# Performance work log

Hardware: AMD Instinct MI355X
Metric: run time of the kernel (lower is better)

## Reference

```python
import jax, jax.numpy as jnp
import numpy as np

N, D, K = 8192, 2048, 10000
EPS = 1e-12
COMMITMENT_COST = 0.25


def _l2_normalize(v, axis):
    # matches torch F.normalize(p=2): v / max(||v||, eps)
    n = jnp.linalg.norm(v, axis=axis, keepdims=True)
    return v / jnp.maximum(n, EPS)


def setup_inputs() -> dict:
    key = jax.random.key(0)
    kx, kw = jax.random.split(key)
    x = jax.random.normal(kx, (N, D), dtype=jnp.float32)
    # nn.Embedding weight initialized uniform(0, 3) per the module
    weight = jax.random.uniform(kw, (K, D), dtype=jnp.float32, minval=0.0, maxval=3.0)
    return {"x": x, "weight": weight}


def reference(x, weight):
    # --- get_code_indices ---
    xn = _l2_normalize(x, axis=1)          # [N, D]
    wn = _l2_normalize(weight, axis=1)     # [K, D]
    # ||xn||^2 + ||wn||^2 - 2 xn . wn  -> [N, K]
    distances = (
        jnp.sum(xn * xn, axis=1, keepdims=True)
        + jnp.sum(wn * wn, axis=1)
        - 2.0 * jnp.matmul(xn, wn.T)
    )
    encoding_indices = jnp.argmin(distances, axis=1)  # [N]
    # --- quantize (gathers the UN-normalized codebook, as in the module) ---
    quantized = weight[encoding_indices]              # [N, D]
    # --- training losses ---
    q_latent_loss = jnp.mean((quantized - jax.lax.stop_gradient(x)) ** 2)
    e_latent_loss = jnp.mean((x - jax.lax.stop_gradient(quantized)) ** 2)
    loss = q_latent_loss + COMMITMENT_COST * e_latent_loss
    # straight-through estimator
    quantized = x + jax.lax.stop_gradient(quantized - x)
    return quantized, loss, encoding_indices
```

## Files before the change

### kernel.cpp

```cpp
#include <hip/hip_runtime.h>
#include <math.h>

typedef unsigned short ushort_t;
typedef short short8 __attribute__((ext_vector_type(8)));
typedef float f32x4  __attribute__((ext_vector_type(4)));

#define N_ROWS 8192
#define D_DIM  2048
#define K_CODES 10000
#define EPSF   1e-12f

#define BMT 256
#define BKT 64
#define NT_K 32
#define MTILES 32
#define NTILES 40
#define NGROUP 320

#define BAND_ADD  2e-5f
#define FBIG 1e30f

__device__ __forceinline__ unsigned short f2bf(float f) {
  unsigned u = __float_as_uint(f);
  unsigned r = (u + 0x7fffu + ((u >> 16) & 1u)) >> 16;
  return (unsigned short)r;
}
__device__ __forceinline__ float bf2f(unsigned short h) {
  return __uint_as_float(((unsigned)h) << 16);
}

__device__ __forceinline__ void stage16(const ushort_t* g, ushort_t* l) {
  __builtin_amdgcn_global_load_lds(
      (const __attribute__((address_space(1))) unsigned int*)g,
      (__attribute__((address_space(3))) unsigned int*)l, 16, 0, 0);
}

__device__ __forceinline__ float block_reduce_sum(float v) {
  #pragma unroll
  for (int o = 32; o > 0; o >>= 1) v += __shfl_down(v, o, 64);
  __shared__ float ls[4];
  int lane = threadIdx.x & 63;
  int wid  = threadIdx.x >> 6;
  if (lane == 0) ls[wid] = v;
  __syncthreads();
  v = (threadIdx.x < 4) ? ls[threadIdx.x] : 0.0f;
  if (wid == 0) {
    v += __shfl_down(v, 2, 64);
    v += __shfl_down(v, 1, 64);
  }
  __syncthreads();
  return v;
}

__global__ __launch_bounds__(256) void norm_hi_kernel(
    const float* __restrict__ src, ushort_t* __restrict__ hi,
    float* __restrict__ sq_out, float* __restrict__ inv_out,
    float* __restrict__ hn_out, float* __restrict__ ln_out)
{
  int row = blockIdx.x;
  int tid = threadIdx.x;
  const float* rp = src + (size_t)row * D_DIM;
  float4 v0 = *(const float4*)(rp + tid * 8);
  float4 v1 = *(const float4*)(rp + tid * 8 + 4);
  float s = v0.x*v0.x + v0.y*v0.y + v0.z*v0.z + v0.w*v0.w
          + v1.x*v1.x + v1.y*v1.y + v1.z*v1.z + v1.w*v1.w;
  s = block_reduce_sum(s);
  __shared__ float sh_inv;
  if (tid == 0) sh_inv = 1.0f / fmaxf(sqrtf(s), EPSF);
  __syncthreads();
  float inv = sh_inv;

  float xs[8] = {v0.x, v0.y, v0.z, v0.w, v1.x, v1.y, v1.z, v1.w};
  unsigned short hb[8];
  float t = 0.0f, th = 0.0f, tl = 0.0f;
  #pragma unroll
  for (int i = 0; i < 8; ++i) {
    float xn = xs[i] * inv;
    t += xn * xn;
    unsigned short h = f2bf(xn);
    hb[i] = h;
    float hf = bf2f(h);
    th += hf * hf;
    float l = xn - hf;
    tl += l * l;
  }
  *(short8*)(hi + (size_t)row * D_DIM + tid * 8) = *(short8*)hb;
  t  = block_reduce_sum(t);
  if (tid == 0) sq_out[row] = t;
  th = block_reduce_sum(th);
  if (tid == 0) hn_out[row] = sqrtf(th);
  tl = block_reduce_sum(tl);
  if (tid == 0) { ln_out[row] = sqrtf(tl); inv_out[row] = inv; }
}

__global__ __launch_bounds__(256) void wmax_kernel(
    const float* __restrict__ whn, const float* __restrict__ wln,
    float* __restrict__ wmax_out)
{
  int tid = threadIdx.x;
  float mh = 0.0f, ml = 0.0f;
  for (int k = tid; k < K_CODES; k += 256) {
    mh = fmaxf(mh, whn[k]);
    ml = fmaxf(ml, wln[k]);
  }
  __shared__ float sh[256], sl[256];
  sh[tid] = mh; sl[tid] = ml;
  __syncthreads();
  #pragma unroll
  for (int o = 128; o > 0; o >>= 1) {
    if (tid < o) {
      sh[tid] = fmaxf(sh[tid], sh[tid + o]);
      sl[tid] = fmaxf(sl[tid], sl[tid + o]);
    }
    __syncthreads();
  }
  if (tid == 0) { wmax_out[0] = sh[0]; wmax_out[1] = sl[0]; }
}

#define LEXLT(da, ia, db, ib) ((da) < (db) || ((da) == (db) && (ia) < (ib)))

#define READ_A(mh) { \
  _Pragma("unroll") for (int mi = 0; mi < 4; ++mi) \
  _Pragma("unroll") for (int kc = 0; kc < 2; ++kc) { \
    int r = (mh)*128 + wr*64 + mi*16 + t16; \
    int sl = (kc*4 + h4) ^ (r & 7); \
    af[mi][kc] = *(const short8*)&lA[buf][r*64 + sl*8]; } }

#define READ_B(nh, DST) { \
  _Pragma("unroll") for (int ni = 0; ni < 2; ++ni) \
  _Pragma("unroll") for (int kc = 0; kc < 2; ++kc) { \
    int r = (nh)*128 + wc*32 + ni*16 + t16; \
    int sl = (kc*4 + h4) ^ (r & 7); \
    DST[ni][kc] = *(const short8*)&lB[buf][r*64 + sl*8]; } }

#define MFMA_Q(mh, nh, BF) { \
  _Pragma("unroll") for (int mi = 0; mi < 4; ++mi) \
  _Pragma("unroll") for (int ni = 0; ni < 2; ++ni) \
  _Pragma("unroll") for (int kc = 0; kc < 2; ++kc) \
    acc[(mh)*4+mi][(nh)*2+ni] = __builtin_amdgcn_mfma_f32_16x16x32_bf16( \
        af[mi][kc], BF[ni][kc], acc[(mh)*4+mi][(nh)*2+ni], 0, 0, 0); }

#define STAGE_A(BF, HH, KKO) { \
  stage16(Ah + (size_t)(row0 + (HH)*128 + prow0) * D_DIM + (KKO) + lsl, \
          lA[BF] + (HH)*8192 + c0*512); \
  stage16(Ah + (size_t)(row0 + (HH)*128 + prow1) * D_DIM + (KKO) + lsl, \
          lA[BF] + (HH)*8192 + c0*512 + 512); }

#define STAGE_B(BF, HH, KKO) { \
  int r0_ = col0 + (HH)*128 + prow0; r0_ = r0_ < K_CODES ? r0_ : K_CODES - 1; \
  int r1_ = col0 + (HH)*128 + prow1; r1_ = r1_ < K_CODES ? r1_ : K_CODES - 1; \
  stage16(Bh + (size_t)r0_ * D_DIM + (KKO) + lsl, \
          lB[BF] + (HH)*8192 + c0*512); \
  stage16(Bh + (size_t)r1_ * D_DIM + (KKO) + lsl, \
          lB[BF] + (HH)*8192 + c0*512 + 512); }

__global__ __launch_bounds__(512, 1) void dist_top2_kernel(
    const ushort_t* __restrict__ Ah, const ushort_t* __restrict__ Bh,
    const float* __restrict__ wsq,
    float* __restrict__ p1d, int* __restrict__ p1i, float* __restrict__ p2d)
{
  __shared__ ushort_t lA[2][16384];
  __shared__ ushort_t lB[2][16384];

  const int tid  = threadIdx.x;
  const int lane = tid & 63;
  const int w8   = tid >> 6;
  const int wr   = w8 >> 2;
  const int wc   = w8 & 3;
  const int t16  = lane & 15;
  const int h4   = lane >> 4;

  int bid = blockIdx.x;
  int xcd = bid & 7, l = bid >> 3;
  int ch = l >> 5;
  int wl = l & 31;
  const int mtile = (xcd & 1) * 16 + (wl & 15);
  const int ntile = (xcd >> 1) * 10 + ch * 2 + (wl >> 4);
  const int row0 = mtile * BMT;
  const int col0 = ntile * BMT;

  const int sub  = lane >> 3;
  const int lsl  = ((lane & 7) ^ sub) * 8;
  const int c0   = w8 * 2;
  const int prow0 = c0 * 8 + sub;
  const int prow1 = prow0 + 8;

  f32x4 acc[8][4];
  #pragma unroll
  for (int m = 0; m < 8; ++m)
    #pragma unroll
    for (int n = 0; n < 4; ++n) acc[m][n] = (f32x4){0.f, 0.f, 0.f, 0.f};

  STAGE_A(0, 0, 0);
  STAGE_B(0, 0, 0);
  STAGE_B(0, 1, 0);
  STAGE_A(0, 1, 0);
  asm volatile("s_waitcnt vmcnt(4)" ::: "memory");
  __builtin_amdgcn_s_barrier();

  short8 af[4][2], bfr0[2][2], bfr1[2][2];

  for (int kt = 0; kt < NT_K; ++kt) {
    const int buf  = kt & 1;
    const int nbuf = buf ^ 1;
    const bool hn  = (kt + 1 < NT_K);
    const int kk = (kt + 1) * BKT;

    READ_A(0);
    READ_B(0, bfr0);
    if (hn) {
      STAGE_A(nbuf, 0, kk);
      asm volatile("s_waitcnt vmcnt(4)" ::: "memory");
    } else {
      asm volatile("s_waitcnt vmcnt(2)" ::: "memory");
    }
    __builtin_amdgcn_s_barrier();
    asm volatile("s_waitcnt lgkmcnt(0)" ::: "memory");
    __builtin_amdgcn_sched_barrier(0);
    __builtin_amdgcn_s_setprio(1);
    MFMA_Q(0, 0, bfr0);
    __builtin_amdgcn_s_setprio(0);
    __builtin_amdgcn_s_barrier();

    READ_B(1, bfr1);
    if (hn) {
      STAGE_B(nbuf, 0, kk);
      asm volatile("s_waitcnt vmcnt(4)" ::: "memory");
    } else {
      asm volatile("s_waitcnt vmcnt(0)" ::: "memory");
    }
    __builtin_amdgcn_s_barrier();
    asm volatile("s_waitcnt lgkmcnt(0)" ::: "memory");
    __builtin_amdgcn_sched_barrier(0);
    __builtin_amdgcn_s_setprio(1);
    MFMA_Q(0, 1, bfr1);
    __builtin_amdgcn_s_setprio(0);
    __builtin_amdgcn_s_barrier();

    READ_A(1);
    if (hn) STAGE_B(nbuf, 1, kk);
    __builtin_amdgcn_s_barrier();
    asm volatile("s_waitcnt lgkmcnt(0)" ::: "memory");
    __builtin_amdgcn_sched_barrier(0);
    __builtin_amdgcn_s_setprio(1);
    MFMA_Q(1, 1, bfr1);
    __builtin_amdgcn_s_setprio(0);
    __builtin_amdgcn_s_barrier();

    if (hn) {
      STAGE_A(nbuf, 1, kk);
      asm volatile("s_waitcnt vmcnt(4)" ::: "memory");
    }
    __builtin_amdgcn_s_barrier();
    __builtin_amdgcn_s_setprio(1);
    MFMA_Q(1, 0, bfr0);
    __builtin_amdgcn_s_setprio(0);
    __builtin_amdgcn_s_barrier();
  }

  float wsqr[4]; int colr[4];
  #pragma unroll
  for (int n = 0; n < 4; ++n) {
    int col = col0 + ((n & 2) ? 128 : 0) + wc * 32 + ((n & 1) ? 16 : 0) + t16;
    colr[n] = col;
    wsqr[n] = (col < K_CODES) ? wsq[col] : FBIG * 10.0f;
  }
  #pragma unroll
  for (int m = 0; m < 8; ++m) {
    int rloc = ((m & 4) ? 128 : 0) + wr * 64 + (m & 3) * 16 + h4 * 4;
    #pragma unroll
    for (int j = 0; j < 4; ++j) {
      #pragma unroll
      for (int half = 0; half < 2; ++half) {
        int na = half * 2, nb = na + 1;
        float da = wsqr[na] - 2.0f * acc[m][na][j]; int ia = colr[na];
        float db = wsqr[nb] - 2.0f * acc[m][nb][j]; int ib = colr[nb];
        float d1, d2; int i1;
        if (LEXLT(db, ib, da, ia)) { d1 = db; i1 = ib; d2 = da; }
        else                       { d1 = da; i1 = ia; d2 = db; }
        #pragma unroll
        for (int off = 1; off < 16; off <<= 1) {
          float od1 = __shfl_xor(d1, off, 64);
          int   oi1 = __shfl_xor(i1, off, 64);
          float od2 = __shfl_xor(d2, off, 64);
          if (LEXLT(od1, oi1, d1, i1)) { d2 = fminf(d1, od2); d1 = od1; i1 = oi1; }
          else                         { d2 = fminf(od1, d2); }
        }
        if (t16 == 0) {
          int grow = row0 + rloc + j;
          int gid = ntile * 8 + half * 4 + wc;
          size_t o = (size_t)grow * NGROUP + gid;
          p1d[o] = d1; p1i[o] = i1; p2d[o] = d2;
        }
      }
    }
  }
}

__global__ __launch_bounds__(256) void refine_kernel(
    const float* __restrict__ x, const float* __restrict__ w,
    const float* __restrict__ xsq, const float* __restrict__ xinv,
    const float* __restrict__ xhn, const float* __restrict__ xln,
    const float* __restrict__ wsq, const float* __restrict__ winv,
    const float* __restrict__ whn, const float* __restrict__ wln,
    const float* __restrict__ wmax,
    const float* __restrict__ p1d, const int* __restrict__ p1i,
    const float* __restrict__ p2d,
    int* __restrict__ idx_out, float* __restrict__ idxf_out)
{
  const int wv   = threadIdx.x >> 6;
  const int lane = threadIdx.x & 63;
  const int row  = blockIdx.x * 4 + wv;

  const float xs = xsq[row], xh = xhn[row], xl = xln[row];
  const float whm = wmax[0], wlm = wmax[1];
  const float eps_max = 2.0f * (xl * whm + xh * wlm + xl * wlm) + BAND_ADD;

  float gd1[5], gd2[5], geps[5];
  int   gi1[5];
  float tmin = FBIG;
  float bmind = FBIG, bmine = 0.0f; int bmink = 0x7fffffff;
  #pragma unroll
  for (int s = 0; s < 5; ++s) {
    size_t o = (size_t)row * NGROUP + lane + 64 * s;
    float d1 = p1d[o]; int i1 = p1i[o]; float d2 = p2d[o];
    int is = i1 < K_CODES ? i1 : K_CODES - 1;
    float e1 = 2.0f * (xl * whn[is] + xh * wln[is] + xl * wln[is]) + BAND_ADD;
    gd1[s] = d1; gi1[s] = i1; gd2[s] = d2; geps[s] = e1;
    tmin = fminf(tmin, d1 + e1);
    if (d1 < bmind || (d1 == bmind && i1 < bmink)) { bmind = d1; bmink = i1; bmine = e1; }
  }
  #pragma unroll
  for (int off = 1; off < 64; off <<= 1) tmin = fminf(tmin, __shfl_xor(tmin, off, 64));
  const float T = tmin;

  #pragma unroll
  for (int off = 1; off < 64; off <<= 1) {
    float od = __shfl_xor(bmind, off, 64);
    int   ok = __shfl_xor(bmink, off, 64);
    if (od < bmind || (od == bmind && ok < bmink)) { bmind = od; bmink = ok; }
  }
  const int kfirst = bmink;

  unsigned long long ms[5], mc[5];
  int ncand = 0, nscan = 0;
  #pragma unroll
  for (int s = 0; s < 5; ++s) {
    bool scan = (gd2[s] - eps_max <= T);
    bool cand = !scan && (gd1[s] - geps[s] <= T);
    ms[s] = __ballot(scan); mc[s] = __ballot(cand);
    nscan += __popcll(ms[s]); ncand += __popcll(mc[s]);
  }
  if (nscan == 0 && ncand == 1) {
    if (lane == 0) { idx_out[row] = kfirst; idxf_out[row] = (float)kfirst; }
    return;
  }

  const float4* xr4 = (const float4*)(x + (size_t)row * D_DIM);
  const float xiv = xinv[row];
  float4 xv[8];
  #pragma unroll
  for (int j = 0; j < 8; ++j) {
    float4 v = xr4[lane + 64 * j];
    v.x *= xiv; v.y *= xiv; v.z *= xiv; v.w *= xiv;
    xv[j] = v;
  }

  float bd = INFINITY; int bi = 0x7fffffff;
  auto refine = [&](int k) {
    const float4* wr4 = (const float4*)(w + (size_t)k * D_DIM);
    const float wiv = winv[k];
    float a = 0.0f;
    #pragma unroll
    for (int j = 0; j < 8; ++j) {
      float4 wvv = wr4[lane + 64 * j];
      a += xv[j].x * (wvv.x * wiv) + xv[j].y * (wvv.y * wiv)
         + xv[j].z * (wvv.z * wiv) + xv[j].w * (wvv.w * wiv);
    }
    #pragma unroll
    for (int off = 32; off > 0; off >>= 1) a += __shfl_xor(a, off, 64);
    float df = (xs + wsq[k]) - 2.0f * a;
    if (df < bd || (df == bd && k < bi)) { bd = df; bi = k; }
  };

  if (kfirst < K_CODES) refine(kfirst);

  #pragma unroll
  for (int s = 0; s < 5; ++s) {
    unsigned long long m = mc[s];
    while (m) {
      int lsrc = __ffsll(m) - 1; m &= m - 1;
      int k = __shfl(gi1[s], lsrc, 64);
      if (k == kfirst || k >= K_CODES) continue;
      float a1d = __shfl(gd1[s],  lsrc, 64);
      float a1e = __shfl(geps[s], lsrc, 64);
      if (a1d - a1e <= bd + BAND_ADD) refine(k);
    }
    m = ms[s];
    while (m) {
      int lsrc = __ffsll(m) - 1; m &= m - 1;
      float a2d = __shfl(gd2[s], lsrc, 64);
      if (a2d - eps_max > bd + BAND_ADD) continue;
      int k0 = (lsrc + 64 * s) * 32;
      for (int kk = 0; kk < 32; ++kk) {
        int k = k0 + kk;
        if (k < K_CODES) refine(k);
      }
    }
  }

  if (lane == 0) { idx_out[row] = bi; idxf_out[row] = (float)bi; }
}

__global__ __launch_bounds__(256) void gather_kernel(
    const float* __restrict__ x, const float* __restrict__ w,
    const int* __restrict__ idx, float* __restrict__ out,
    float* __restrict__ lpart)
{
  int row = blockIdx.x;
  int tid = threadIdx.x;
  int id = idx[row];
  const float4* wr_ = (const float4*)(w + (size_t)id * D_DIM);
  const float4* xr  = (const float4*)(x + (size_t)row * D_DIM);
  float4* outr = (float4*)(out + (size_t)row * D_DIM);
  float s = 0.0f;
  #pragma unroll
  for (int t = 0; t < 2; ++t) {
    int e = tid + t * 256;
    float4 wv = wr_[e], xv = xr[e];
    outr[e] = wv;
    float d0 = wv.x - xv.x, d1 = wv.y - xv.y, d2 = wv.z - xv.z, d3 = wv.w - xv.w;
    s += d0 * d0 + d1 * d1 + d2 * d2 + d3 * d3;
  }
  s = block_reduce_sum(s);
  if (tid == 0) lpart[row] = s;
}

__global__ __launch_bounds__(256) void loss_kernel(const float* __restrict__ lpart,
                                                   float* __restrict__ loss_out)
{
  int tid = threadIdx.x;
  double s = 0.0;
  for (int t = tid; t < N_ROWS; t += 256) s += (double)lpart[t];
  __shared__ double sd[256];
  sd[tid] = s;
  __syncthreads();
  #pragma unroll
  for (int o = 128; o > 0; o >>= 1) {
    if (tid < o) sd[tid] += sd[tid + o];
    __syncthreads();
  }
  if (tid == 0)
    loss_out[0] = (float)(1.25 * sd[0] / (double)((size_t)N_ROWS * (size_t)D_DIM));
}

extern "C" void kernel_launch(void* const* d_in, const int* in_sizes, int n_in,
                              void* d_out, int out_size, void* d_ws, size_t ws_size,
                              hipStream_t stream) {
  const float* x = (const float*)d_in[0];
  const float* w = (const float*)d_in[1];
  float* out = (float*)d_out;
  char*  ws  = (char*)d_ws;

  size_t off = 0;
  auto alloc = [&](size_t bytes) {
    size_t o = off;
    off = (off + bytes + 255) & ~(size_t)255;
    return o;
  };
  const size_t szA1 = (size_t)N_ROWS * D_DIM * 2;
  const size_t szB1 = (size_t)K_CODES * D_DIM * 2;
  const size_t szP  = (size_t)NGROUP * N_ROWS * 4;

  ushort_t* Bh = (ushort_t*)(ws + alloc(szB1));
  float* wsq  = (float*)(ws + alloc((size_t)K_CODES * 4));
  float* winv = (float*)(ws + alloc((size_t)K_CODES * 4));
  float* whn  = (float*)(ws + alloc((size_t)K_CODES * 4));
  float* wln  = (float*)(ws + alloc((size_t)K_CODES * 4));
  float* wmax = (float*)(ws + alloc(2 * 4));
  float* xsq  = (float*)(ws + alloc((size_t)N_ROWS * 4));
  float* xinv = (float*)(ws + alloc((size_t)N_ROWS * 4));
  float* xhn  = (float*)(ws + alloc((size_t)N_ROWS * 4));
  float* xln  = (float*)(ws + alloc((size_t)N_ROWS * 4));
  float* p1d  = (float*)(ws + alloc(szP));
  int*   p1i  = (int*)  (ws + alloc(szP));
  float* p2d  = (float*)(ws + alloc(szP));
  int*   idx  = (int*)  (ws + alloc((size_t)N_ROWS * 4));
  float* lpart = (float*)(ws + alloc((size_t)N_ROWS * 4));

  ushort_t* Ahp;
  if (ws_size >= off + szA1) {
    Ahp = (ushort_t*)(ws + alloc(szA1));
  } else {
    Ahp = (ushort_t*)out;
  }

  float* loss_out = out + (size_t)N_ROWS * D_DIM;
  float* idxf_out = loss_out + 1;

  norm_hi_kernel<<<N_ROWS, 256, 0, stream>>>(x, Ahp, xsq, xinv, xhn, xln);
  norm_hi_kernel<<<K_CODES, 256, 0, stream>>>(w, Bh, wsq, winv, whn, wln);
  wmax_kernel<<<1, 256, 0, stream>>>(whn, wln, wmax);
  dist_top2_kernel<<<MTILES * NTILES, 512, 0, stream>>>(
      Ahp, Bh, wsq, p1d, p1i, p2d);
  refine_kernel<<<N_ROWS / 4, 256, 0, stream>>>(
      x, w, xsq, xinv, xhn, xln, wsq, winv, whn, wln, wmax,
      p1d, p1i, p2d, idx, idxf_out);
  gather_kernel<<<N_ROWS, 256, 0, stream>>>(x, w, idx, out, lpart);
  loss_kernel<<<1, 256, 0, stream>>>(lpart, loss_out);
}
```

Before: 783.5 us.

## Simplify GEMM main loop to stage-all-then-compute with one barrier per tile

Replaces the hand-interleaved main loop of the distance GEMM with a simpler schedule. Previously it had four sub-phases, each with its own global→LDS stage, explicit vmcnt/lgkmcnt waits and paired barriers. Now all next-tile stages are issued at the top of each iteration, the four MFMA quadrants run back to back, and a single __syncthreads closes the iteration. LDS read addresses are precomputed as per-thread base pointers, and launch_bounds is raised to 2 blocks per CU, which mainly tightens the register budget because 128KB of LDS per block likely still limits occupancy. The aim is to cut barrier and wait overhead, at the risk of worse latency hiding and register spills of the 128-float accumulator.

```diff
diff --git a/kernel.cpp b/kernel.cpp
--- a/kernel.cpp
+++ b/kernel.cpp
@@ -119,19 +119,16 @@
 
 #define LEXLT(da, ia, db, ib) ((da) < (db) || ((da) == (db) && (ia) < (ib)))
 
+
 #define READ_A(mh) { \
-  _Pragma("unroll") for (int mi = 0; mi < 4; ++mi) \
-  _Pragma("unroll") for (int kc = 0; kc < 2; ++kc) { \
-    int r = (mh)*128 + wr*64 + mi*16 + t16; \
-    int sl = (kc*4 + h4) ^ (r & 7); \
-    af[mi][kc] = *(const short8*)&lA[buf][r*64 + sl*8]; } }
+  _Pragma("unroll") for (int mi = 0; mi < 4; ++mi) { \
+    af[mi][0] = *(const short8*)(aP0 + bo + (mh)*8192 + mi*1024); \
+    af[mi][1] = *(const short8*)(aP1 + bo + (mh)*8192 + mi*1024); } }
 
 #define READ_B(nh, DST) { \
-  _Pragma("unroll") for (int ni = 0; ni < 2; ++ni) \
-  _Pragma("unroll") for (int kc = 0; kc < 2; ++kc) { \
-    int r = (nh)*128 + wc*32 + ni*16 + t16; \
-    int sl = (kc*4 + h4) ^ (r & 7); \
-    DST[ni][kc] = *(const short8*)&lB[buf][r*64 + sl*8]; } }
+  _Pragma("unroll") for (int ni = 0; ni < 2; ++ni) { \
+    DST[ni][0] = *(const short8*)(bP0 + bo + (nh)*8192 + ni*1024); \
+    DST[ni][1] = *(const short8*)(bP1 + bo + (nh)*8192 + ni*1024); } }
 
 #define MFMA_Q(mh, nh, BF) { \
   _Pragma("unroll") for (int mi = 0; mi < 4; ++mi) \
@@ -140,21 +137,21 @@
     acc[(mh)*4+mi][(nh)*2+ni] = __builtin_amdgcn_mfma_f32_16x16x32_bf16( \
         af[mi][kc], BF[ni][kc], acc[(mh)*4+mi][(nh)*2+ni], 0, 0, 0); }
 
-#define STAGE_A(BF, HH, KKO) { \
+#define STAGE_A(NB, HH, KKO) { \
   stage16(Ah + (size_t)(row0 + (HH)*128 + prow0) * D_DIM + (KKO) + lsl, \
-          lA[BF] + (HH)*8192 + c0*512); \
+          &lA[0][0] + (NB)*16384 + (HH)*8192 + c0*512); \
   stage16(Ah + (size_t)(row0 + (HH)*128 + prow1) * D_DIM + (KKO) + lsl, \
-          lA[BF] + (HH)*8192 + c0*512 + 512); }
-
-#define STAGE_B(BF, HH, KKO) { \
+          &lA[0][0] + (NB)*16384 + (HH)*8192 + c0*512 + 512); }
+
+#define STAGE_B(NB, HH, KKO) { \
   int r0_ = col0 + (HH)*128 + prow0; r0_ = r0_ < K_CODES ? r0_ : K_CODES - 1; \
   int r1_ = col0 + (HH)*128 + prow1; r1_ = r1_ < K_CODES ? r1_ : K_CODES - 1; \
   stage16(Bh + (size_t)r0_ * D_DIM + (KKO) + lsl, \
-          lB[BF] + (HH)*8192 + c0*512); \
+          &lB[0][0] + (NB)*16384 + (HH)*8192 + c0*512); \
   stage16(Bh + (size_t)r1_ * D_DIM + (KKO) + lsl, \
-          lB[BF] + (HH)*8192 + c0*512 + 512); }
-
-__global__ __launch_bounds__(512, 1) void dist_top2_kernel(
+          &lB[0][0] + (NB)*16384 + (HH)*8192 + c0*512 + 512); }
+
+__global__ __launch_bounds__(512, 2) void dist_top2_kernel(
     const ushort_t* __restrict__ Ah, const ushort_t* __restrict__ Bh,
     const float* __restrict__ wsq,
     float* __restrict__ p1d, int* __restrict__ p1i, float* __restrict__ p2d)
@@ -185,6 +182,13 @@
   const int prow0 = c0 * 8 + sub;
   const int prow1 = prow0 + 8;
 
+  const int rA = wr * 64 + t16;
+  const ushort_t* aP0 = &lA[0][rA * 64 + ((h4     ^ (rA & 7)) * 8)];
+  const ushort_t* aP1 = &lA[0][rA * 64 + (((4+h4) ^ (rA & 7)) * 8)];
+  const int rB = wc * 32 + t16;
+  const ushort_t* bP0 = &lB[0][rB * 64 + ((h4     ^ (rB & 7)) * 8)];
+  const ushort_t* bP1 = &lB[0][rB * 64 + (((4+h4) ^ (rB & 7)) * 8)];
+
   f32x4 acc[8][4];
   #pragma unroll
   for (int m = 0; m < 8; ++m)
@@ -195,67 +199,39 @@
   STAGE_B(0, 0, 0);
   STAGE_B(0, 1, 0);
   STAGE_A(0, 1, 0);
-  asm volatile("s_waitcnt vmcnt(4)" ::: "memory");
-  __builtin_amdgcn_s_barrier();
+  __syncthreads();
 
   short8 af[4][2], bfr0[2][2], bfr1[2][2];
 
   for (int kt = 0; kt < NT_K; ++kt) {
-    const int buf  = kt & 1;
-    const int nbuf = buf ^ 1;
+    const int bo   = (kt & 1) * 16384;
+    const int nb   = (kt + 1) & 1;
     const bool hn  = (kt + 1 < NT_K);
-    const int kk = (kt + 1) * BKT;
+    const int kk   = (kt + 1) * BKT;
+
+    if (hn) {
+      STAGE_A(nb, 0, kk);
+      STAGE_B(nb, 0, kk);
+      STAGE_B(nb, 1, kk);
+      STAGE_A(nb, 1, kk);
+    }
 
     READ_A(0);
     READ_B(0, bfr0);
-    if (hn) {
-      STAGE_A(nbuf, 0, kk);
-      asm volatile("s_waitcnt vmcnt(4)" ::: "memory");
-    } else {
-      asm volatile("s_waitcnt vmcnt(2)" ::: "memory");
-    }
-    __builtin_amdgcn_s_barrier();
-    asm volatile("s_waitcnt lgkmcnt(0)" ::: "memory");
-    __builtin_amdgcn_sched_barrier(0);
     __builtin_amdgcn_s_setprio(1);
     MFMA_Q(0, 0, bfr0);
     __builtin_amdgcn_s_setprio(0);
-    __builtin_amdgcn_s_barrier();
-
     READ_B(1, bfr1);
-    if (hn) {
-      STAGE_B(nbuf, 0, kk);
-      asm volatile("s_waitcnt vmcnt(4)" ::: "memory");
-    } else {
-      asm volatile("s_waitcnt vmcnt(0)" ::: "memory");
-    }
-    __builtin_amdgcn_s_barrier();
-    asm volatile("s_waitcnt lgkmcnt(0)" ::: "memory");
-    __builtin_amdgcn_sched_barrier(0);
     __builtin_amdgcn_s_setprio(1);
     MFMA_Q(0, 1, bfr1);
     __builtin_amdgcn_s_setprio(0);
-    __builtin_amdgcn_s_barrier();
-
     READ_A(1);
-    if (hn) STAGE_B(nbuf, 1, kk);
-    __builtin_amdgcn_s_barrier();
-    asm volatile("s_waitcnt lgkmcnt(0)" ::: "memory");
-    __builtin_amdgcn_sched_barrier(0);
     __builtin_amdgcn_s_setprio(1);
     MFMA_Q(1, 1, bfr1);
-    __builtin_amdgcn_s_setprio(0);
-    __builtin_amdgcn_s_barrier();
-
-    if (hn) {
-      STAGE_A(nbuf, 1, kk);
-      asm volatile("s_waitcnt vmcnt(4)" ::: "memory");
-    }
-    __builtin_amdgcn_s_barrier();
-    __builtin_amdgcn_s_setprio(1);
     MFMA_Q(1, 0, bfr0);
     __builtin_amdgcn_s_setprio(0);
-    __builtin_amdgcn_s_barrier();
+
+    __syncthreads();
   }
 
   float wsqr[4]; int colr[4];
@@ -272,9 +248,9 @@
     for (int j = 0; j < 4; ++j) {
       #pragma unroll
       for (int half = 0; half < 2; ++half) {
-        int na = half * 2, nb = na + 1;
-        float da = wsqr[na] - 2.0f * acc[m][na][j]; int ia = colr[na];
-        float db = wsqr[nb] - 2.0f * acc[m][nb][j]; int ib = colr[nb];
+        int na = half * 2, nb2 = na + 1;
+        float da = wsqr[na]  - 2.0f * acc[m][na][j];  int ia = colr[na];
+        float db = wsqr[nb2] - 2.0f * acc[m][nb2][j]; int ib = colr[nb2];
         float d1, d2; int i1;
         if (LEXLT(db, ib, da, ia)) { d1 = db; i1 = ib; d2 = da; }
         else                       { d1 = da; i1 = ia; d2 = db; }
@@ -319,7 +295,7 @@
   float gd1[5], gd2[5], geps[5];
   int   gi1[5];
   float tmin = FBIG;
-  float bmind = FBIG, bmine = 0.0f; int bmink = 0x7fffffff;
+  float bmind = FBIG; int bmink = 0x7fffffff;
   #pragma unroll
   for (int s = 0; s < 5; ++s) {
     size_t o = (size_t)row * NGROUP + lane + 64 * s;
@@ -328,7 +304,7 @@
     float e1 = 2.0f * (xl * whn[is] + xh * wln[is] + xl * wln[is]) + BAND_ADD;
     gd1[s] = d1; gi1[s] = i1; gd2[s] = d2; geps[s] = e1;
     tmin = fminf(tmin, d1 + e1);
-    if (d1 < bmind || (d1 == bmind && i1 < bmink)) { bmind = d1; bmink = i1; bmine = e1; }
+    if (d1 < bmind || (d1 == bmind && i1 < bmink)) { bmind = d1; bmink = i1; }
   }
   #pragma unroll
   for (int off = 1; off < 64; off <<= 1) tmin = fminf(tmin, __shfl_xor(tmin, off, 64));
```

After: 785.5 us. About the same (+0.3%).
